# Kernel optimization log

Measured on AMD Instinct MI355X. Metric: run time of the kernel, lower is better.

Reference implementation:

```python
import jax, jax.numpy as jnp
import numpy as np

DIM = 768
HEAD = 12
DK = DIM // HEAD

def setup_inputs() -> dict:
    key = jax.random.key(0)
    ks = jax.random.split(key, 9)
    B, L = 4, 2048
    s = 1.0 / np.sqrt(DIM)
    qkv = jax.random.normal(ks[0], (B, L, DIM), dtype=jnp.float32)
    mask = jnp.ones((B, L), dtype=jnp.int32)
    Wq = jax.random.normal(ks[1], (DIM, DIM), dtype=jnp.float32) * s
    bq = jnp.zeros((DIM,), dtype=jnp.float32)
    Wk = jax.random.normal(ks[2], (DIM, DIM), dtype=jnp.float32) * s
    bk = jnp.zeros((DIM,), dtype=jnp.float32)
    Wv = jax.random.normal(ks[3], (DIM, DIM), dtype=jnp.float32) * s
    bv = jnp.zeros((DIM,), dtype=jnp.float32)
    Wo = jax.random.normal(ks[4], (DIM, DIM), dtype=jnp.float32) * s
    bo = jnp.zeros((DIM,), dtype=jnp.float32)
    return {"qkv": qkv, "mask": mask, "Wq": Wq, "bq": bq, "Wk": Wk, "bk": bk,
            "Wv": Wv, "bv": bv, "Wo": Wo, "bo": bo}

def reference(qkv, mask, Wq, bq, Wk, bk, Wv, bv, Wo, bo):
    B, L, _ = qkv.shape
    def proj(W, b):
        # [B,L,dim] -> [B,H,L,dk]
        return (qkv @ W + b).reshape(B, L, HEAD, DK).transpose(0, 2, 1, 3)
    q, k, v = proj(Wq, bq), proj(Wk, bk), proj(Wv, bv)
    scores = jnp.einsum('bhqd,bhkd->bhqk', q, k) / jnp.sqrt(jnp.float32(DK))
    # mask: [B,L] broadcast over heads and query positions (key axis)
    m = mask[:, None, None, :]  # [B,1,1,L]
    scores = jnp.where(m == 0, jnp.float32(-1e9), scores)
    p = jax.nn.softmax(scores, axis=-1)
    x = jnp.einsum('bhqk,bhkd->bhqd', p, v)  # [B,H,L,dk]
    x = x.transpose(0, 2, 1, 3).reshape(B, L, DIM)
    return x @ Wo + bo
```

## Files before the change

### kernel.cpp

```cpp
#include <hip/hip_runtime.h>
#include <hip/hip_bf16.h>
#include <stdint.h>

#define DIM  768
#define NHEAD 12
#define DK   64
#define BATCH 4
#define SEQ  2048
#define ROWS (BATCH*SEQ)
#define SCL  0.1803368801111204f

typedef __bf16 bf16_t;
typedef bf16_t bf16x8 __attribute__((ext_vector_type(8)));
typedef bf16_t bf16x4 __attribute__((ext_vector_type(4)));
typedef float  f32x4  __attribute__((ext_vector_type(4)));
typedef float  f32x16 __attribute__((ext_vector_type(16)));

typedef unsigned int __attribute__((address_space(1)))* as1p;
typedef unsigned int __attribute__((address_space(3)))* as3p;

__device__ __forceinline__ void gload_lds16(const void* g, void* l) {
    __builtin_amdgcn_global_load_lds((as1p)g, (as3p)l, 16, 0, 0);
}
#define MEMFENCE asm volatile("" ::: "memory")

__global__ void cast_bf16_kernel(const float* __restrict__ in, bf16_t* __restrict__ out) {
    int i = blockIdx.x * 256 + threadIdx.x;
    const float4* p = (const float4*)in;
    float4 a = p[(size_t)i*2], b = p[(size_t)i*2+1];
    bf16x8 v;
    v[0]=(bf16_t)a.x; v[1]=(bf16_t)a.y; v[2]=(bf16_t)a.z; v[3]=(bf16_t)a.w;
    v[4]=(bf16_t)b.x; v[5]=(bf16_t)b.y; v[6]=(bf16_t)b.z; v[7]=(bf16_t)b.w;
    *(bf16x8*)(out + (size_t)i*8) = v;
}

__global__ void wtrans_kernel(const float* __restrict__ W0, const float* __restrict__ W1,
                              const float* __restrict__ W2, const float* __restrict__ W3,
                              bf16_t* __restrict__ T0, bf16_t* __restrict__ T1,
                              bf16_t* __restrict__ T2, bf16_t* __restrict__ T3) {
    const float* W = blockIdx.z==0?W0 : blockIdx.z==1?W1 : blockIdx.z==2?W2 : W3;
    bf16_t*      T = blockIdx.z==0?T0 : blockIdx.z==1?T1 : blockIdx.z==2?T2 : T3;
    __shared__ float tile[32][33];
    int tx = threadIdx.x, ty = threadIdx.y;
    int c = blockIdx.x*32 + tx;
    #pragma unroll
    for (int r = 0; r < 32; r += 8)
        tile[ty+r][tx] = W[(size_t)(blockIdx.y*32 + ty + r)*DIM + c];
    __syncthreads();
    int oc = blockIdx.y*32 + tx;
    #pragma unroll
    for (int r = 0; r < 32; r += 8)
        T[(size_t)(blockIdx.x*32 + ty + r)*DIM + oc] = (bf16_t)tile[tx][ty+r];
}

template<int MODE>
__global__ __launch_bounds__(256) void gemm_kernel(
    const bf16_t* __restrict__ A,
    const bf16_t* __restrict__ WTa, const bf16_t* __restrict__ WTb, const bf16_t* __restrict__ WTc,
    const float* __restrict__ ba, const float* __restrict__ bb, const float* __restrict__ bc,
    bf16_t* __restrict__ Qo, bf16_t* __restrict__ Ko, bf16_t* __restrict__ Vo,
    float* __restrict__ Oo) {
    __shared__ __align__(16) bf16_t As[128*64];
    __shared__ __align__(16) bf16_t Bs[128*64];
    const int tid = threadIdx.x, wave = tid>>6, lane = tid&63;
    const int wm = wave>>1, wn = wave&1;
    const int m0 = blockIdx.x*128, n0 = blockIdx.y*128;
    const int z = (MODE==0) ? (int)blockIdx.z : 0;
    const bf16_t* WT  = (z==0) ? WTa : (z==1 ? WTb : WTc);
    const float* bias = (z==0) ? ba  : (z==1 ? bb  : bc);

    f32x4 acc[4][4];
    const f32x4 zf = {0.f,0.f,0.f,0.f};
    #pragma unroll
    for (int m = 0; m < 4; ++m)
        #pragma unroll
        for (int n = 0; n < 4; ++n) acc[m][n] = zf;

    const int srow = wave*32 + (lane>>3);
    const int scol = (lane&7)*8;
    const bf16_t* Ag = A  + (size_t)(m0+srow)*DIM + scol;
    const bf16_t* Bg = WT + (size_t)(n0+srow)*DIM + scol;
    bf16_t* AsW = As + (wave*32)*64;
    bf16_t* BsW = Bs + (wave*32)*64;

    for (int k0 = 0; k0 < DIM; k0 += 64) {
        __syncthreads();
        #pragma unroll
        for (int i = 0; i < 4; ++i) {
            gload_lds16(Ag + (size_t)(i*8)*DIM + k0, AsW + i*8*64);
            gload_lds16(Bg + (size_t)(i*8)*DIM + k0, BsW + i*8*64);
        }
        __syncthreads();
        #pragma unroll
        for (int ks = 0; ks < 2; ++ks) {
            bf16x8 af[4], bfr[4];
            #pragma unroll
            for (int m = 0; m < 4; ++m)
                af[m]  = *(const bf16x8*)&As[(wm*64 + m*16 + (lane&15))*64 + ks*32 + (lane>>4)*8];
            #pragma unroll
            for (int n = 0; n < 4; ++n)
                bfr[n] = *(const bf16x8*)&Bs[(wn*64 + n*16 + (lane&15))*64 + ks*32 + (lane>>4)*8];
            #pragma unroll
            for (int m = 0; m < 4; ++m)
                #pragma unroll
                for (int n = 0; n < 4; ++n)
                    acc[m][n] = __builtin_amdgcn_mfma_f32_16x16x32_bf16(af[m], bfr[n], acc[m][n], 0, 0, 0);
        }
    }

    float bvv[4];
    #pragma unroll
    for (int n = 0; n < 4; ++n) bvv[n] = bias[n0 + wn*64 + n*16 + (lane&15)];

    #pragma unroll
    for (int m = 0; m < 4; ++m) {
        #pragma unroll
        for (int n = 0; n < 4; ++n) {
            #pragma unroll
            for (int r = 0; r < 4; ++r) {
                float val = acc[m][n][r] + bvv[n];
                int R = m0 + wm*64 + m*16 + (lane>>4)*4 + r;
                int C = n0 + wn*64 + n*16 + (lane&15);
                if (MODE == 1) {
                    Oo[(size_t)R*DIM + C] = val;
                } else {
                    int bi = R>>11, li = R&2047, h = C>>6, d = C&63;
                    size_t bh = (size_t)(bi*NHEAD + h);
                    if      (z==0) Qo[(bh*SEQ + li)*DK + d] = (bf16_t)(val*SCL);
                    else if (z==1) Ko[(bh*SEQ + li)*DK + d] = (bf16_t)val;
                    else {
                        int li2 = (li & ~12) | ((li&4)<<1) | ((li&8)>>1);
                        Vo[(bh*DK + d)*SEQ + li2] = (bf16_t)val;
                    }
                }
            }
        }
    }
}

#define NT (SEQ/64)

__global__ __launch_bounds__(256) void attn_kernel(
    const bf16_t* __restrict__ Q, const bf16_t* __restrict__ K, const bf16_t* __restrict__ VT,
    const int* __restrict__ mask, bf16_t* __restrict__ X) {
    __shared__ __align__(16) bf16_t lds[2*8192];
    const int tid = threadIdx.x, wv = tid>>6, lane = tid&63;
    const int lo5 = lane&31, hi5 = lane>>5;
    const int b = blockIdx.x;
    const int xcd = b & 7, ii = b >> 3;
    const int bh = xcd*6 + (ii>>4), qt = ii & 15;
    const int bi = bh/NHEAD, h = bh%NHEAD;
    const bf16_t* Qb = Q  + (size_t)bh*SEQ*DK;
    const bf16_t* Kb = K  + (size_t)bh*SEQ*DK;
    const bf16_t* Vb = VT + (size_t)bh*DK*SEQ;
    const int* mk = mask + (size_t)bi*SEQ + lo5;
    const int q0 = qt*128 + wv*32;

    int mOk = 1;
    {
        const int4* m4 = (const int4*)(mask + (size_t)bi*SEQ);
        #pragma unroll
        for (int i2 = 0; i2 < 8; ++i2) {
            int4 v = m4[lane + i2*64];
            mOk &= (v.x != 0) & (v.y != 0) & (v.z != 0) & (v.w != 0);
        }
    }
    const int mAll = __all(mOk);

    bf16x8 qf[4];
    #pragma unroll
    for (int ks = 0; ks < 4; ++ks)
        qf[ks] = *(const bf16x8*)&Qb[(size_t)(q0 + lo5)*DK + ks*16 + hi5*8];

    f32x16 O0, O1;
    #pragma unroll
    for (int r = 0; r < 16; ++r) { O0[r] = 0.f; O1[r] = 0.f; }
    float lsum = 0.f;

    bf16x8 onesb = {};
    if (hi5 == 0) onesb[0] = (bf16_t)1.0f;

    const int srow  = wv*16 + (lane>>3);
    const int sslot = (lane&7) ^ (srow&7);
    const bf16_t* Kg = Kb + (size_t)srow*DK  + sslot*8;
    const bf16_t* Vg = Vb + (size_t)srow*SEQ + sslot*8;
    int koff[4];
    #pragma unroll
    for (int ks = 0; ks < 4; ++ks) koff[ks] = (((2*ks + hi5) ^ (lo5 & 7)) << 3);

    #pragma unroll
    for (int i = 0; i < 2; ++i) {
        gload_lds16(Kg + (size_t)(i*8)*DK,  lds +        (wv*16 + i*8)*64);
        gload_lds16(Vg + (size_t)(i*8)*SEQ, lds + 4096 + (wv*16 + i*8)*64);
    }

    int cur = 0;
    for (int t = 0; t < NT; ++t) {
        const int kv0 = t*64;
        if (t < NT-1) {
            bf16_t* nb = lds + (cur^1)*8192;
            #pragma unroll
            for (int i = 0; i < 2; ++i) {
                gload_lds16(Kg + (size_t)(kv0+64)*DK + (size_t)(i*8)*DK,  nb +        (wv*16 + i*8)*64);
                gload_lds16(Vg + (kv0+64)            + (size_t)(i*8)*SEQ, nb + 4096 + (wv*16 + i*8)*64);
            }
            asm volatile("s_waitcnt vmcnt(4)" ::: "memory");
        } else {
            asm volatile("s_waitcnt vmcnt(0)" ::: "memory");
        }
        MEMFENCE; __builtin_amdgcn_s_barrier(); MEMFENCE;

        const bf16_t* Kt = lds + cur*8192;
        const bf16_t* Vt = lds + cur*8192 + 4096;

        f32x16 s0, s1;
        #pragma unroll
        for (int r = 0; r < 16; ++r) { s0[r] = -12.f; s1[r] = -12.f; }
        #pragma unroll
        for (int ks = 0; ks < 4; ++ks) {
            bf16x8 a0 = *(const bf16x8*)&Kt[ lo5     *64 + koff[ks]];
            bf16x8 a1 = *(const bf16x8*)&Kt[(32+lo5)*64 + koff[ks]];
            s0 = __builtin_amdgcn_mfma_f32_32x32x16_bf16(a0, qf[ks], s0, 0, 0, 0);
            s1 = __builtin_amdgcn_mfma_f32_32x32x16_bf16(a1, qf[ks], s1, 0, 0, 0);
        }
        if (!mAll) {
            int mv0 = mk[kv0], mv1 = mk[kv0 + 32];
            bf16x8 ba = {};
            ba[0] = mv0 ? (bf16_t)0.f : (bf16_t)(-1024.0f);
            s0 = __builtin_amdgcn_mfma_f32_32x32x16_bf16(ba, onesb, s0, 0, 0, 0);
            ba[0] = mv1 ? (bf16_t)0.f : (bf16_t)(-1024.0f);
            s1 = __builtin_amdgcn_mfma_f32_32x32x16_bf16(ba, onesb, s1, 0, 0, 0);
        }

        #pragma unroll
        for (int r = 0; r < 16; ++r) {
            s0[r] = __builtin_amdgcn_exp2f(s0[r]);
            s1[r] = __builtin_amdgcn_exp2f(s1[r]);
        }
        float t01[16];
        #pragma unroll
        for (int r = 0; r < 16; ++r) t01[r] = s0[r] + s1[r];
        float u[8];
        #pragma unroll
        for (int r = 0; r < 8; ++r) u[r] = t01[r] + t01[r+8];
        float w0 = (u[0]+u[1]) + (u[2]+u[3]);
        float w1 = (u[4]+u[5]) + (u[6]+u[7]);
        float ps = w0 + w1;
        lsum += ps + __shfl_xor(ps, 32);

        bf16x8 pf0, pf1, pf2, pf3;
        #pragma unroll
        for (int j = 0; j < 8; ++j) {
            pf0[j] = (bf16_t)s0[j];
            pf1[j] = (bf16_t)s0[8+j];
            pf2[j] = (bf16_t)s1[j];
            pf3[j] = (bf16_t)s1[8+j];
        }

        #pragma unroll
        for (int ks = 0; ks < 4; ++ks) {
            bf16x8 pb = (ks==0) ? pf0 : (ks==1) ? pf1 : (ks==2) ? pf2 : pf3;
            bf16x8 a0 = *(const bf16x8*)&Vt[ lo5     *64 + koff[ks]];
            bf16x8 a1 = *(const bf16x8*)&Vt[(32+lo5)*64 + koff[ks]];
            O0 = __builtin_amdgcn_mfma_f32_32x32x16_bf16(a0, pb, O0, 0, 0, 0);
            O1 = __builtin_amdgcn_mfma_f32_32x32x16_bf16(a1, pb, O1, 0, 0, 0);
        }
        MEMFENCE; __builtin_amdgcn_s_barrier(); MEMFENCE;
        cur ^= 1;
    }

    float rl = __builtin_amdgcn_rcpf(lsum);
    const size_t rowb = (size_t)(bi*SEQ + q0 + lo5)*DIM + h*DK;
    #pragma unroll
    for (int g = 0; g < 4; ++g) {
        bf16x4 v0, v1;
        #pragma unroll
        for (int j = 0; j < 4; ++j) {
            v0[j] = (bf16_t)(O0[g*4+j] * rl);
            v1[j] = (bf16_t)(O1[g*4+j] * rl);
        }
        *(bf16x4*)&X[rowb + g*8 + hi5*4]      = v0;
        *(bf16x4*)&X[rowb + 32 + g*8 + hi5*4] = v1;
    }
}

extern "C" void kernel_launch(void* const* d_in, const int* in_sizes, int n_in,
                              void* d_out, int out_size, void* d_ws, size_t ws_size,
                              hipStream_t stream) {
    (void)in_sizes; (void)n_in; (void)out_size; (void)ws_size;
    const float* qkv = (const float*)d_in[0];
    const int*  mask = (const int*)d_in[1];
    const float* Wq = (const float*)d_in[2];
    const float* bq = (const float*)d_in[3];
    const float* Wk = (const float*)d_in[4];
    const float* bk = (const float*)d_in[5];
    const float* Wv = (const float*)d_in[6];
    const float* bv = (const float*)d_in[7];
    const float* Wo = (const float*)d_in[8];
    const float* bo = (const float*)d_in[9];
    float* out = (float*)d_out;

    char* ws = (char*)d_ws;
    size_t off = 0;
    auto carve = [&](size_t bytes) { void* p = ws + off; off += (bytes + 255) & ~(size_t)255; return p; };
    const size_t actN = (size_t)ROWS*DIM;
    bf16_t* Abf = (bf16_t*)carve(actN*2);
    bf16_t* WTq = (bf16_t*)carve((size_t)DIM*DIM*2);
    bf16_t* WTk = (bf16_t*)carve((size_t)DIM*DIM*2);
    bf16_t* WTv = (bf16_t*)carve((size_t)DIM*DIM*2);
    bf16_t* WTo = (bf16_t*)carve((size_t)DIM*DIM*2);
    bf16_t* Qb  = (bf16_t*)carve(actN*2);
    bf16_t* Kb  = (bf16_t*)carve(actN*2);
    bf16_t* VTb = (bf16_t*)carve(actN*2);
    bf16_t* Xb  = (bf16_t*)carve(actN*2);

    cast_bf16_kernel<<<dim3(ROWS*DIM/8/256), dim3(256), 0, stream>>>(qkv, Abf);
    wtrans_kernel<<<dim3(24,24,4), dim3(32,8), 0, stream>>>(Wq, Wk, Wv, Wo, WTq, WTk, WTv, WTo);
    gemm_kernel<0><<<dim3(64,6,3), dim3(256), 0, stream>>>(Abf, WTq, WTk, WTv, bq, bk, bv,
                                                           Qb, Kb, VTb, nullptr);
    attn_kernel<<<dim3(768), dim3(256), 0, stream>>>(Qb, Kb, VTb, mask, Xb);
    gemm_kernel<1><<<dim3(64,6,1), dim3(256), 0, stream>>>(Xb, WTo, WTo, WTo, bo, bo, bo,
                                                           nullptr, nullptr, nullptr, out);
}
```

Measured before the change: 179.9 us.

## Double-buffer GEMM LDS tiles and remap blocks for XCD-local L2 reuse

The projection GEMMs now use two LDS buffers, so the global-to-LDS load of the next K tile is issued before the MFMA work on the current one. Explicit vmcnt waits and raw s_barriers replace the old syncthreads pairs. The grid is flattened to 1D and block indices are remapped so each XCD handles a contiguous band of M tiles across all N tiles and Q/K/V outputs, aiming to improve L2 reuse of A rows. LDS use doubles to 64KB per block, which may reduce occupancy.

```diff
diff --git a/kernel.cpp b/kernel.cpp
--- a/kernel.cpp
+++ b/kernel.cpp
@@ -60,12 +60,16 @@
     const float* __restrict__ ba, const float* __restrict__ bb, const float* __restrict__ bc,
     bf16_t* __restrict__ Qo, bf16_t* __restrict__ Ko, bf16_t* __restrict__ Vo,
     float* __restrict__ Oo) {
-    __shared__ __align__(16) bf16_t As[128*64];
-    __shared__ __align__(16) bf16_t Bs[128*64];
+    __shared__ __align__(16) bf16_t As[2][128*64];
+    __shared__ __align__(16) bf16_t Bs[2][128*64];
     const int tid = threadIdx.x, wave = tid>>6, lane = tid&63;
     const int wm = wave>>1, wn = wave&1;
-    const int m0 = blockIdx.x*128, n0 = blockIdx.y*128;
-    const int z = (MODE==0) ? (int)blockIdx.z : 0;
+    const int b = blockIdx.x;
+    const int xcd = b & 7, ib = b >> 3;
+    int z, ntile, mtile;
+    if (MODE == 0) { z = ib % 3; ntile = (ib/3) % 6; mtile = xcd*8 + ib/18; }
+    else           { z = 0;      ntile = ib % 6;     mtile = xcd*8 + ib/6;  }
+    const int m0 = mtile*128, n0 = ntile*128;
     const bf16_t* WT  = (z==0) ? WTa : (z==1 ? WTb : WTc);
     const float* bias = (z==0) ? ba  : (z==1 ? bb  : bc);
 
@@ -80,32 +84,46 @@
     const int scol = (lane&7)*8;
     const bf16_t* Ag = A  + (size_t)(m0+srow)*DIM + scol;
     const bf16_t* Bg = WT + (size_t)(n0+srow)*DIM + scol;
-    bf16_t* AsW = As + (wave*32)*64;
-    bf16_t* BsW = Bs + (wave*32)*64;
-
-    for (int k0 = 0; k0 < DIM; k0 += 64) {
-        __syncthreads();
-        #pragma unroll
-        for (int i = 0; i < 4; ++i) {
-            gload_lds16(Ag + (size_t)(i*8)*DIM + k0, AsW + i*8*64);
-            gload_lds16(Bg + (size_t)(i*8)*DIM + k0, BsW + i*8*64);
-        }
-        __syncthreads();
+    const int woff = (wave*32)*64;
+
+    #pragma unroll
+    for (int i2 = 0; i2 < 4; ++i2) {
+        gload_lds16(Ag + (size_t)(i2*8)*DIM, &As[0][woff + i2*8*64]);
+        gload_lds16(Bg + (size_t)(i2*8)*DIM, &Bs[0][woff + i2*8*64]);
+    }
+
+    int cur = 0;
+    for (int t = 0; t < DIM/64; ++t) {
+        if (t < DIM/64 - 1) {
+            const size_t k1 = (size_t)(t+1)*64;
+            #pragma unroll
+            for (int i2 = 0; i2 < 4; ++i2) {
+                gload_lds16(Ag + (size_t)(i2*8)*DIM + k1, &As[cur^1][woff + i2*8*64]);
+                gload_lds16(Bg + (size_t)(i2*8)*DIM + k1, &Bs[cur^1][woff + i2*8*64]);
+            }
+            asm volatile("s_waitcnt vmcnt(8)" ::: "memory");
+        } else {
+            asm volatile("s_waitcnt vmcnt(0)" ::: "memory");
+        }
+        MEMFENCE; __builtin_amdgcn_s_barrier(); MEMFENCE;
+
         #pragma unroll
         for (int ks = 0; ks < 2; ++ks) {
             bf16x8 af[4], bfr[4];
             #pragma unroll
             for (int m = 0; m < 4; ++m)
-                af[m]  = *(const bf16x8*)&As[(wm*64 + m*16 + (lane&15))*64 + ks*32 + (lane>>4)*8];
+                af[m]  = *(const bf16x8*)&As[cur][(wm*64 + m*16 + (lane&15))*64 + ks*32 + (lane>>4)*8];
             #pragma unroll
             for (int n = 0; n < 4; ++n)
-                bfr[n] = *(const bf16x8*)&Bs[(wn*64 + n*16 + (lane&15))*64 + ks*32 + (lane>>4)*8];
+                bfr[n] = *(const bf16x8*)&Bs[cur][(wn*64 + n*16 + (lane&15))*64 + ks*32 + (lane>>4)*8];
             #pragma unroll
             for (int m = 0; m < 4; ++m)
                 #pragma unroll
                 for (int n = 0; n < 4; ++n)
                     acc[m][n] = __builtin_amdgcn_mfma_f32_16x16x32_bf16(af[m], bfr[n], acc[m][n], 0, 0, 0);
         }
+        MEMFENCE; __builtin_amdgcn_s_barrier(); MEMFENCE;
+        cur ^= 1;
     }
 
     float bvv[4];
@@ -316,9 +334,9 @@
 
     cast_bf16_kernel<<<dim3(ROWS*DIM/8/256), dim3(256), 0, stream>>>(qkv, Abf);
     wtrans_kernel<<<dim3(24,24,4), dim3(32,8), 0, stream>>>(Wq, Wk, Wv, Wo, WTq, WTk, WTv, WTo);
-    gemm_kernel<0><<<dim3(64,6,3), dim3(256), 0, stream>>>(Abf, WTq, WTk, WTv, bq, bk, bv,
-                                                           Qb, Kb, VTb, nullptr);
+    gemm_kernel<0><<<dim3(1152), dim3(256), 0, stream>>>(Abf, WTq, WTk, WTv, bq, bk, bv,
+                                                         Qb, Kb, VTb, nullptr);
     attn_kernel<<<dim3(768), dim3(256), 0, stream>>>(Qb, Kb, VTb, mask, Xb);
-    gemm_kernel<1><<<dim3(64,6,1), dim3(256), 0, stream>>>(Xb, WTo, WTo, WTo, bo, bo, bo,
-                                                           nullptr, nullptr, nullptr, out);
-}
+    gemm_kernel<1><<<dim3(384), dim3(256), 0, stream>>>(Xb, WTo, WTo, WTo, bo, bo, bo,
+                                                        nullptr, nullptr, nullptr, out);
+}
```

New measurement: 168.8 us, median of 3. 1.07x faster.
